# Optimization experiments

Measured on AMD Instinct MI355X. Metric: run time of the kernel, lower is better.

## Reference

```python
import jax, jax.numpy as jnp
import numpy as np

B, S, H, D = 4, 2048, 16, 64
E = H * D  # embed_dim = 1024


def setup_inputs() -> dict:
    key = jax.random.key(0)
    kq, kk, kv, kw, kb = jax.random.split(key, 5)
    query = jax.random.normal(kq, (B, S, H, D), dtype=jnp.float32)
    key_t = jax.random.normal(kk, (B, S, H, D), dtype=jnp.float32)
    value = jax.random.normal(kv, (B, S, H, D), dtype=jnp.float32)
    qkv_proj = jnp.zeros((1,), dtype=jnp.float32)  # unused arg in original forward
    # causal mask (0 = masked), matching masked_fill(attn_mask == 0, -inf)
    attn_mask = jnp.tril(jnp.ones((S, S), dtype=jnp.int32))
    bound = 1.0 / np.sqrt(E)
    out_w = jax.random.uniform(kw, (E, E), jnp.float32, -bound, bound)
    out_b = jax.random.uniform(kb, (E,), jnp.float32, -bound, bound)
    return {"query": query, "key": key_t, "value": value, "qkv_proj": qkv_proj,
            "attn_mask": attn_mask, "out_w": out_w, "out_b": out_b}


def reference(query, key, value, qkv_proj, attn_mask, out_w, out_b):
    # flatten heads: module does single-head attention over embed_dim
    q = query.reshape(B, S, E) * (float(E) ** -0.5)  # scaling uses embed_dim, per source
    k = key.reshape(B, S, E)
    v = value.reshape(B, S, E)
    scores = jnp.einsum('bqe,bke->bqk', q, k)  # [B,S,S]
    scores = jnp.where(attn_mask[None, :, :] == 0, -jnp.inf, scores)
    # safe softmax: subtract max, exp, normalize
    probs = jax.nn.softmax(scores, axis=-1)
    attn_out = jnp.einsum('bqk,bke->bqe', probs, v)  # [B,S,E]
    return attn_out @ out_w.T + out_b
```

## Files before the change

kernel.cpp:

```cpp
#include <hip/hip_runtime.h>


typedef __attribute__((ext_vector_type(8))) short bf16x8;
typedef __attribute__((ext_vector_type(4))) float floatx4;

#define MFMA16(a, b, c) __builtin_amdgcn_mfma_f32_16x16x32_bf16((a), (b), (c), 0, 0, 0)

#define B_ 4
#define S_ 2048
#define E_ 1024

static __device__ __forceinline__ unsigned short f2bf(float f) {
  unsigned int u = __float_as_uint(f);
  u += 0x7FFFu + ((u >> 16) & 1u);
  return (unsigned short)(u >> 16);
}

#define STAGE_TILE(dst, srcbase, LD, k0, w, l, NITER)                          \
  _Pragma("unroll")                                                            \
  for (int i_ = 0; i_ < (NITER); ++i_) {                                       \
    int c_ = i_ * 256 + (w) * 64 + (l);                                        \
    int row_ = c_ >> 3, cg_ = c_ & 7;                                          \
    int col_ = (cg_ ^ (row_ & 7)) * 8;                                         \
    __builtin_amdgcn_global_load_lds(                                          \
        (const __attribute__((address_space(1))) unsigned int*)((srcbase) +    \
            (size_t)row_ * (LD) + (k0) + col_),                                \
        (__attribute__((address_space(3))) unsigned int*)((dst) +              \
            (size_t)(i_ * 256 + (w) * 64) * 8),                                \
        16, 0, 0);                                                             \
  }
#define STAGE_TILE_64(dst, srcbase, LD, k0, w, l) STAGE_TILE(dst, srcbase, LD, k0, w, l, 4)

static __device__ __forceinline__ const bf16x8* frag_at(
    const unsigned short* base, int row, int cg) {
  return (const bf16x8*)(base + (size_t)row * 64 + ((cg ^ (row & 7)) * 8));
}

static __device__ __forceinline__ void cvt8(const float* __restrict__ src,
                                            unsigned short* __restrict__ dst,
                                            float sc) {
  float4 x0 = *(const float4*)src;
  float4 x1 = *(const float4*)(src + 4);
  bf16x8 o;
  o[0] = f2bf(x0.x * sc); o[1] = f2bf(x0.y * sc);
  o[2] = f2bf(x0.z * sc); o[3] = f2bf(x0.w * sc);
  o[4] = f2bf(x1.x * sc); o[5] = f2bf(x1.y * sc);
  o[6] = f2bf(x1.z * sc); o[7] = f2bf(x1.w * sc);
  *(bf16x8*)dst = o;
}

__global__ __launch_bounds__(256) void cvt_qk_kernel(
    const float* __restrict__ Q, const float* __restrict__ K,
    unsigned short* __restrict__ Qbf, unsigned short* __restrict__ Kbf) {
  const int bid = blockIdx.x;
  const int qside = bid < 4096;
  const size_t i8 = ((size_t)(qside ? bid : bid - 4096) * 256 + threadIdx.x) * 8;
  if (qside) cvt8(Q + i8, Qbf + i8, 0.03125f);
  else       cvt8(K + i8, Kbf + i8, 1.0f);
}

__global__ __launch_bounds__(256, 4) void qk_cvtvw_kernel(
    const unsigned short* __restrict__ A,
    const unsigned short* __restrict__ Bw,
    unsigned short* __restrict__ SP,
    float* __restrict__ rsp,
    const float* __restrict__ V, const float* __restrict__ W,
    unsigned short* __restrict__ Vbf, unsigned short* __restrict__ Wbf) {
  __shared__ unsigned short At[128 * 64];
  __shared__ unsigned short Bt[128 * 64];
  __shared__ float rs_l[2][128];
  const int bid0 = blockIdx.x;

  if (bid0 >= 544) {
    const int t = (bid0 - 544) * 256 + threadIdx.x;
#pragma unroll
    for (int k = 0; k < 8; ++k) {
      int u = t + k * 147456;
      if (u < 1048576) {
        cvt8(V + (size_t)u * 8, Vbf + (size_t)u * 8, 1.0f);
      } else {
        size_t uw = (size_t)(u - 1048576) * 8;
        cvt8(W + uw, Wbf + uw, 1.0f);
      }
    }
    return;
  }

  const int bid = (bid0 & 7) * 68 + (bid0 >> 3);
  const int b = bid / 136;
  const int ti = bid - b * 136;
  float fr = sqrtf(8.0f * (float)ti + 1.0f);
  int trow = (int)((fr - 1.0f) * 0.5f);
  if ((trow + 1) * (trow + 2) / 2 <= ti) ++trow;
  else if (trow * (trow + 1) / 2 > ti) --trow;
  const int tcol = ti - trow * (trow + 1) / 2;
  const int bm = trow * 128, bn = tcol * 128;

  const int tid = threadIdx.x;
  const int w = tid >> 6, l = tid & 63;
  const int l15 = l & 15, l4 = l >> 4;
  const int wr = w >> 1, wc = w & 1;
  const unsigned short* Ab = A + (size_t)b * S_ * E_ + (size_t)bm * E_;
  const unsigned short* Bb = Bw + (size_t)b * S_ * E_ + (size_t)bn * E_;

  floatx4 acc[4][4];
#pragma unroll
  for (int m = 0; m < 4; ++m)
#pragma unroll
    for (int n = 0; n < 4; ++n) acc[m][n] = (floatx4)0.0f;

  for (int k0 = 0; k0 < E_; k0 += 64) {
    STAGE_TILE_64(At, Ab, E_, k0, w, l)
    STAGE_TILE_64(Bt, Bb, E_, k0, w, l)
    __syncthreads();
#pragma unroll
    for (int h = 0; h < 2; ++h) {
      bf16x8 af[4], bfv[4];
#pragma unroll
      for (int mf = 0; mf < 4; ++mf)
        af[mf] = *frag_at(At, wr * 64 + mf * 16 + l15, h * 4 + l4);
#pragma unroll
      for (int nf = 0; nf < 4; ++nf)
        bfv[nf] = *frag_at(Bt, wc * 64 + nf * 16 + l15, h * 4 + l4);
#pragma unroll
      for (int mf = 0; mf < 4; ++mf)
#pragma unroll
        for (int nf = 0; nf < 4; ++nf)
          acc[mf][nf] = MFMA16(af[mf], bfv[nf], acc[mf][nf]);
    }
    __syncthreads();
  }

  float ps[16];
#pragma unroll
  for (int i = 0; i < 16; ++i) ps[i] = 0.0f;
  unsigned short* Cb = SP + (size_t)b * S_ * S_;
#pragma unroll
  for (int mf = 0; mf < 4; ++mf)
#pragma unroll
    for (int nf = 0; nf < 4; ++nf)
#pragma unroll
      for (int r = 0; r < 4; ++r) {
        int row = bm + wr * 64 + mf * 16 + l4 * 4 + r;
        int col = bn + wc * 64 + nf * 16 + l15;
        float p = (col <= row) ? __expf(acc[mf][nf][r]) : 0.0f;
        ps[mf * 4 + r] += p;
        Cb[(size_t)row * S_ + col] = f2bf(p);
      }
#pragma unroll
  for (int i = 0; i < 16; ++i) {
    float s = ps[i];
    s += __shfl_xor(s, 1);
    s += __shfl_xor(s, 2);
    s += __shfl_xor(s, 4);
    s += __shfl_xor(s, 8);
    ps[i] = s;
  }
  if (l15 == 0) {
#pragma unroll
    for (int mf = 0; mf < 4; ++mf)
#pragma unroll
      for (int r = 0; r < 4; ++r)
        rs_l[wc][wr * 64 + mf * 16 + l4 * 4 + r] = ps[mf * 4 + r];
  }
  __syncthreads();
  if (tid < 128)
    rsp[((size_t)(b * S_ + bm + tid)) * 17 + tcol] = rs_l[0][tid] + rs_l[1][tid];
}

__global__ __launch_bounds__(256, 3) void vw_kernel(
    const unsigned short* __restrict__ Wbf,
    const unsigned short* __restrict__ Vbf,
    unsigned short* __restrict__ Ut) {
  __shared__ unsigned short At[128 * 64];
  __shared__ unsigned short Bt[128 * 64];
  const int bid0 = blockIdx.x;
  const int bid = (bid0 & 7) * 64 + (bid0 >> 3);
  const int b = bid >> 7;
  const int mt = (bid >> 4) & 7;
  const int nt = bid & 15;
  const int bm = mt * 128, bn = nt * 128;

  const int tid = threadIdx.x;
  const int w = tid >> 6, l = tid & 63;
  const int l15 = l & 15, l4 = l >> 4;
  const int wr = w >> 1, wc = w & 1;
  const unsigned short* Ab = Wbf + (size_t)bm * E_;
  const unsigned short* Bb = Vbf + (size_t)b * S_ * E_ + (size_t)bn * E_;

  floatx4 acc[4][4];
#pragma unroll
  for (int m = 0; m < 4; ++m)
#pragma unroll
    for (int n = 0; n < 4; ++n) acc[m][n] = (floatx4)0.0f;

  for (int k0 = 0; k0 < E_; k0 += 64) {
    STAGE_TILE_64(At, Ab, E_, k0, w, l)
    STAGE_TILE_64(Bt, Bb, E_, k0, w, l)
    __syncthreads();
#pragma unroll
    for (int h = 0; h < 2; ++h) {
      bf16x8 af[4], bfv[4];
#pragma unroll
      for (int mf = 0; mf < 4; ++mf)
        af[mf] = *frag_at(At, wr * 64 + mf * 16 + l15, h * 4 + l4);
#pragma unroll
      for (int nf = 0; nf < 4; ++nf)
        bfv[nf] = *frag_at(Bt, wc * 64 + nf * 16 + l15, h * 4 + l4);
#pragma unroll
      for (int mf = 0; mf < 4; ++mf)
#pragma unroll
        for (int nf = 0; nf < 4; ++nf)
          acc[mf][nf] = MFMA16(af[mf], bfv[nf], acc[mf][nf]);
    }
    __syncthreads();
  }

  unsigned short* Cb = Ut + (size_t)b * E_ * S_;
#pragma unroll
  for (int mf = 0; mf < 4; ++mf)
#pragma unroll
    for (int nf = 0; nf < 4; ++nf)
#pragma unroll
      for (int r = 0; r < 4; ++r) {
        int row = bm + wr * 64 + mf * 16 + l4 * 4 + r;
        int col = bn + wc * 64 + nf * 16 + l15;
        Cb[(size_t)row * S_ + col] = f2bf(acc[mf][nf][r]);
      }
}

__global__ __launch_bounds__(256, 4) void pu_kernel(
    const unsigned short* __restrict__ P,
    const unsigned short* __restrict__ Ut,
    const float* __restrict__ rsp,
    const float* __restrict__ bias,
    float* __restrict__ out) {
  __shared__ unsigned short At[128 * 64];
  __shared__ unsigned short Bt[64 * 64];
  __shared__ float inv_l[128];
  const int bid0 = blockIdx.x;
  const int x = bid0 & 7;
  const int j = bid0 >> 3;
  const int b = x >> 1;
  const int nt = (x & 1) * 8 + (j & 7);
  const int r2 = j >> 3;
  const int mt = (r2 < 8) ? r2 : 23 - r2;
  const int bm = mt * 128, bn = nt * 64;

  const int tid = threadIdx.x;
  const int w = tid >> 6, l = tid & 63;
  const int l15 = l & 15, l4 = l >> 4;
  const int wr = w >> 1, wc = w & 1;

  {
    float* srd = (float*)At;
    const float4* rp4 =
        (const float4*)(rsp + ((size_t)(b * S_ + bm)) * 17);
    for (int i = tid; i < 544; i += 256) ((float4*)srd)[i] = rp4[i];
    __syncthreads();
    if (tid < 128) {
      float s = 0.0f;
      for (int t = 0; t <= mt; ++t) s += srd[tid * 17 + t];
      inv_l[tid] = 1.0f / s;
    }
    __syncthreads();
  }

  const unsigned short* Ab = P + (size_t)b * S_ * S_ + (size_t)bm * S_;
  const unsigned short* Bb = Ut + (size_t)b * E_ * S_ + (size_t)bn * S_;

  floatx4 acc[4][2];
#pragma unroll
  for (int m = 0; m < 4; ++m)
#pragma unroll
    for (int n = 0; n < 2; ++n) acc[m][n] = (floatx4)0.0f;

  const int kmax = (mt + 1) * 128;
  for (int k0 = 0; k0 < kmax; k0 += 64) {
    STAGE_TILE(At, Ab, S_, k0, w, l, 4)
    STAGE_TILE(Bt, Bb, S_, k0, w, l, 2)
    __syncthreads();
#pragma unroll
    for (int h = 0; h < 2; ++h) {
      bf16x8 af[4], bfv[2];
#pragma unroll
      for (int mf = 0; mf < 4; ++mf)
        af[mf] = *frag_at(At, wr * 64 + mf * 16 + l15, h * 4 + l4);
#pragma unroll
      for (int nf = 0; nf < 2; ++nf)
        bfv[nf] = *frag_at(Bt, wc * 32 + nf * 16 + l15, h * 4 + l4);
#pragma unroll
      for (int mf = 0; mf < 4; ++mf)
#pragma unroll
        for (int nf = 0; nf < 2; ++nf)
          acc[mf][nf] = MFMA16(af[mf], bfv[nf], acc[mf][nf]);
    }
    __syncthreads();
  }

  float* Cb = out + (size_t)b * S_ * E_;
  float bv[2];
#pragma unroll
  for (int nf = 0; nf < 2; ++nf) bv[nf] = bias[bn + wc * 32 + nf * 16 + l15];
#pragma unroll
  for (int mf = 0; mf < 4; ++mf) {
    float inv[4];
#pragma unroll
    for (int r = 0; r < 4; ++r)
      inv[r] = inv_l[wr * 64 + mf * 16 + l4 * 4 + r];
#pragma unroll
    for (int nf = 0; nf < 2; ++nf)
#pragma unroll
      for (int r = 0; r < 4; ++r) {
        int row = bm + wr * 64 + mf * 16 + l4 * 4 + r;
        int col = bn + wc * 32 + nf * 16 + l15;
        Cb[(size_t)row * E_ + col] = acc[mf][nf][r] * inv[r] + bv[nf];
      }
  }
}

extern "C" void kernel_launch(void* const* d_in, const int* in_sizes, int n_in,
                              void* d_out, int out_size, void* d_ws, size_t ws_size,
                              hipStream_t stream) {
  const float* Q    = (const float*)d_in[0];
  const float* Kf   = (const float*)d_in[1];
  const float* V    = (const float*)d_in[2];
  const float* W    = (const float*)d_in[5];
  const float* bias = (const float*)d_in[6];
  float* out = (float*)d_out;
  (void)ws_size;

  char* ws = (char*)d_ws;
  unsigned short* Qbf = (unsigned short*)(ws);
  unsigned short* Kbf = (unsigned short*)(ws + (size_t)(16u << 20));
  unsigned short* Vbf = (unsigned short*)(ws + (size_t)(32u << 20));
  unsigned short* Wbf = (unsigned short*)(ws + (size_t)(48u << 20));
  unsigned short* SP  = (unsigned short*)(ws + (size_t)(50u << 20));
  float*          rsp = (float*)(ws + (size_t)(82u << 20));
  unsigned short* Ut = Qbf;

  cvt_qk_kernel<<<8192, 256, 0, stream>>>(Q, Kf, Qbf, Kbf);
  qk_cvtvw_kernel<<<544 + 576, 256, 0, stream>>>(Qbf, Kbf, SP, rsp,
                                                 V, W, Vbf, Wbf);
  vw_kernel<<<512, 256, 0, stream>>>(Wbf, Vbf, Ut);
  pu_kernel<<<1024, 256, 0, stream>>>(SP, Ut, rsp, bias, out);
}
```

Measured before the change: 99.92 us.

## Reorder pipeline: convert V/W first, overlap Q/K conversion with VW GEMM

Reorders the kernel sequence so that V and W are converted first. The V·W GEMM then runs alongside the Q/K fp32-to-bf16 conversion blocks in one launch, and the QK GEMM becomes a standalone kernel. Ut moves to its own workspace region instead of aliasing Qbf. The aim is a better pairing of memory-bound conversion with compute, at the cost of a larger workspace footprint and a different balance of conversion versus GEMM blocks per launch.

New measurement: 99.19 us, median of 2. About the same (-0.7%).

```diff
diff --git a/kernel.cpp b/kernel.cpp
--- a/kernel.cpp
+++ b/kernel.cpp
@@ -29,7 +29,6 @@
             (size_t)(i_ * 256 + (w) * 64) * 8),                                \
         16, 0, 0);                                                             \
   }
-#define STAGE_TILE_64(dst, srcbase, LD, k0, w, l) STAGE_TILE(dst, srcbase, LD, k0, w, l, 4)
 
 static __device__ __forceinline__ const bf16x8* frag_at(
     const unsigned short* base, int row, int cg) {
@@ -49,43 +48,104 @@
   *(bf16x8*)dst = o;
 }
 
-__global__ __launch_bounds__(256) void cvt_qk_kernel(
+__global__ __launch_bounds__(256) void cvt_vw_kernel(
+    const float* __restrict__ V, const float* __restrict__ W,
+    unsigned short* __restrict__ Vbf, unsigned short* __restrict__ Wbf) {
+  const int bid = blockIdx.x;
+  const int vside = bid < 4096;
+  const size_t i8 = ((size_t)(vside ? bid : bid - 4096) * 256 + threadIdx.x) * 8;
+  if (vside) cvt8(V + i8, Vbf + i8, 1.0f);
+  else       cvt8(W + i8, Wbf + i8, 1.0f);
+}
+
+__global__ __launch_bounds__(256, 3) void vw_cvtqk_kernel(
+    const unsigned short* __restrict__ Wbf,
+    const unsigned short* __restrict__ Vbf,
+    unsigned short* __restrict__ Ut,
     const float* __restrict__ Q, const float* __restrict__ K,
     unsigned short* __restrict__ Qbf, unsigned short* __restrict__ Kbf) {
-  const int bid = blockIdx.x;
-  const int qside = bid < 4096;
-  const size_t i8 = ((size_t)(qside ? bid : bid - 4096) * 256 + threadIdx.x) * 8;
-  if (qside) cvt8(Q + i8, Qbf + i8, 0.03125f);
-  else       cvt8(K + i8, Kbf + i8, 1.0f);
-}
-
-__global__ __launch_bounds__(256, 4) void qk_cvtvw_kernel(
+  __shared__ unsigned short At[128 * 64];
+  __shared__ unsigned short Bt[128 * 64];
+  const int bid0 = blockIdx.x;
+
+  if (bid0 >= 512) {
+    const int t = (bid0 - 512) * 256 + threadIdx.x;
+#pragma unroll
+    for (int k = 0; k < 8; ++k) {
+      int u = t + k * 262144;
+      if (u < 1048576) {
+        cvt8(Q + (size_t)u * 8, Qbf + (size_t)u * 8, 0.03125f);
+      } else {
+        size_t uk = (size_t)(u - 1048576) * 8;
+        cvt8(K + uk, Kbf + uk, 1.0f);
+      }
+    }
+    return;
+  }
+
+  const int bid = (bid0 & 7) * 64 + (bid0 >> 3);
+  const int b = bid >> 7;
+  const int mt = (bid >> 4) & 7;
+  const int nt = bid & 15;
+  const int bm = mt * 128, bn = nt * 128;
+
+  const int tid = threadIdx.x;
+  const int w = tid >> 6, l = tid & 63;
+  const int l15 = l & 15, l4 = l >> 4;
+  const int wr = w >> 1, wc = w & 1;
+  const unsigned short* Ab = Wbf + (size_t)bm * E_;
+  const unsigned short* Bb = Vbf + (size_t)b * S_ * E_ + (size_t)bn * E_;
+
+  floatx4 acc[4][4];
+#pragma unroll
+  for (int m = 0; m < 4; ++m)
+#pragma unroll
+    for (int n = 0; n < 4; ++n) acc[m][n] = (floatx4)0.0f;
+
+  for (int k0 = 0; k0 < E_; k0 += 64) {
+    STAGE_TILE(At, Ab, E_, k0, w, l, 4)
+    STAGE_TILE(Bt, Bb, E_, k0, w, l, 4)
+    __syncthreads();
+#pragma unroll
+    for (int h = 0; h < 2; ++h) {
+      bf16x8 af[4], bfv[4];
+#pragma unroll
+      for (int mf = 0; mf < 4; ++mf)
+        af[mf] = *frag_at(At, wr * 64 + mf * 16 + l15, h * 4 + l4);
+#pragma unroll
+      for (int nf = 0; nf < 4; ++nf)
+        bfv[nf] = *frag_at(Bt, wc * 64 + nf * 16 + l15, h * 4 + l4);
+#pragma unroll
+      for (int mf = 0; mf < 4; ++mf)
+#pragma unroll
+        for (int nf = 0; nf < 4; ++nf)
+          acc[mf][nf] = MFMA16(af[mf], bfv[nf], acc[mf][nf]);
+    }
+    __syncthreads();
+  }
+
+  unsigned short* Cb = Ut + (size_t)b * E_ * S_;
+#pragma unroll
+  for (int mf = 0; mf < 4; ++mf)
+#pragma unroll
+    for (int nf = 0; nf < 4; ++nf)
+#pragma unroll
+      for (int r = 0; r < 4; ++r) {
+        int row = bm + wr * 64 + mf * 16 + l4 * 4 + r;
+        int col = bn + wc * 64 + nf * 16 + l15;
+        Cb[(size_t)row * S_ + col] = f2bf(acc[mf][nf][r]);
+      }
+}
+
+__global__ __launch_bounds__(256, 4) void qk_kernel(
     const unsigned short* __restrict__ A,
     const unsigned short* __restrict__ Bw,
     unsigned short* __restrict__ SP,
-    float* __restrict__ rsp,
-    const float* __restrict__ V, const float* __restrict__ W,
-    unsigned short* __restrict__ Vbf, unsigned short* __restrict__ Wbf) {
+    float* __restrict__ rsp) {
   __shared__ unsigned short At[128 * 64];
   __shared__ unsigned short Bt[128 * 64];
   __shared__ float rs_l[2][128];
   const int bid0 = blockIdx.x;
-
-  if (bid0 >= 544) {
-    const int t = (bid0 - 544) * 256 + threadIdx.x;
-#pragma unroll
-    for (int k = 0; k < 8; ++k) {
-      int u = t + k * 147456;
-      if (u < 1048576) {
-        cvt8(V + (size_t)u * 8, Vbf + (size_t)u * 8, 1.0f);
-      } else {
-        size_t uw = (size_t)(u - 1048576) * 8;
-        cvt8(W + uw, Wbf + uw, 1.0f);
-      }
-    }
-    return;
-  }
-
   const int bid = (bid0 & 7) * 68 + (bid0 >> 3);
   const int b = bid / 136;
   const int ti = bid - b * 136;
@@ -110,8 +170,8 @@
     for (int n = 0; n < 4; ++n) acc[m][n] = (floatx4)0.0f;
 
   for (int k0 = 0; k0 < E_; k0 += 64) {
-    STAGE_TILE_64(At, Ab, E_, k0, w, l)
-    STAGE_TILE_64(Bt, Bb, E_, k0, w, l)
+    STAGE_TILE(At, Ab, E_, k0, w, l, 4)
+    STAGE_TILE(Bt, Bb, E_, k0, w, l, 4)
     __syncthreads();
 #pragma unroll
     for (int h = 0; h < 2; ++h) {
@@ -166,67 +226,6 @@
   __syncthreads();
   if (tid < 128)
     rsp[((size_t)(b * S_ + bm + tid)) * 17 + tcol] = rs_l[0][tid] + rs_l[1][tid];
-}
-
-__global__ __launch_bounds__(256, 3) void vw_kernel(
-    const unsigned short* __restrict__ Wbf,
-    const unsigned short* __restrict__ Vbf,
-    unsigned short* __restrict__ Ut) {
-  __shared__ unsigned short At[128 * 64];
-  __shared__ unsigned short Bt[128 * 64];
-  const int bid0 = blockIdx.x;
-  const int bid = (bid0 & 7) * 64 + (bid0 >> 3);
-  const int b = bid >> 7;
-  const int mt = (bid >> 4) & 7;
-  const int nt = bid & 15;
-  const int bm = mt * 128, bn = nt * 128;
-
-  const int tid = threadIdx.x;
-  const int w = tid >> 6, l = tid & 63;
-  const int l15 = l & 15, l4 = l >> 4;
-  const int wr = w >> 1, wc = w & 1;
-  const unsigned short* Ab = Wbf + (size_t)bm * E_;
-  const unsigned short* Bb = Vbf + (size_t)b * S_ * E_ + (size_t)bn * E_;
-
-  floatx4 acc[4][4];
-#pragma unroll
-  for (int m = 0; m < 4; ++m)
-#pragma unroll
-    for (int n = 0; n < 4; ++n) acc[m][n] = (floatx4)0.0f;
-
-  for (int k0 = 0; k0 < E_; k0 += 64) {
-    STAGE_TILE_64(At, Ab, E_, k0, w, l)
-    STAGE_TILE_64(Bt, Bb, E_, k0, w, l)
-    __syncthreads();
-#pragma unroll
-    for (int h = 0; h < 2; ++h) {
-      bf16x8 af[4], bfv[4];
-#pragma unroll
-      for (int mf = 0; mf < 4; ++mf)
-        af[mf] = *frag_at(At, wr * 64 + mf * 16 + l15, h * 4 + l4);
-#pragma unroll
-      for (int nf = 0; nf < 4; ++nf)
-        bfv[nf] = *frag_at(Bt, wc * 64 + nf * 16 + l15, h * 4 + l4);
-#pragma unroll
-      for (int mf = 0; mf < 4; ++mf)
-#pragma unroll
-        for (int nf = 0; nf < 4; ++nf)
-          acc[mf][nf] = MFMA16(af[mf], bfv[nf], acc[mf][nf]);
-    }
-    __syncthreads();
-  }
-
-  unsigned short* Cb = Ut + (size_t)b * E_ * S_;
-#pragma unroll
-  for (int mf = 0; mf < 4; ++mf)
-#pragma unroll
-    for (int nf = 0; nf < 4; ++nf)
-#pragma unroll
-      for (int r = 0; r < 4; ++r) {
-        int row = bm + wr * 64 + mf * 16 + l4 * 4 + r;
-        int col = bn + wc * 64 + nf * 16 + l15;
-        Cb[(size_t)row * S_ + col] = f2bf(acc[mf][nf][r]);
-      }
 }
 
 __global__ __launch_bounds__(256, 4) void pu_kernel(
@@ -337,11 +336,11 @@
   unsigned short* Wbf = (unsigned short*)(ws + (size_t)(48u << 20));
   unsigned short* SP  = (unsigned short*)(ws + (size_t)(50u << 20));
   float*          rsp = (float*)(ws + (size_t)(82u << 20));
-  unsigned short* Ut = Qbf;
-
-  cvt_qk_kernel<<<8192, 256, 0, stream>>>(Q, Kf, Qbf, Kbf);
-  qk_cvtvw_kernel<<<544 + 576, 256, 0, stream>>>(Qbf, Kbf, SP, rsp,
-                                                 V, W, Vbf, Wbf);
-  vw_kernel<<<512, 256, 0, stream>>>(Wbf, Vbf, Ut);
+  unsigned short* Ut  = (unsigned short*)(ws + (size_t)(84u << 20));
+
+  cvt_vw_kernel<<<4608, 256, 0, stream>>>(V, W, Vbf, Wbf);
+  vw_cvtqk_kernel<<<512 + 1024, 256, 0, stream>>>(Wbf, Vbf, Ut,
+                                                  Q, Kf, Qbf, Kbf);
+  qk_kernel<<<544, 256, 0, stream>>>(Qbf, Kbf, SP, rsp);
   pu_kernel<<<1024, 256, 0, stream>>>(SP, Ut, rsp, bias, out);
 }
```
